# Performance work log

Hardware: AMD Instinct MI355X
Metric: run time of the kernel (lower is better)

## Reference

```python
import jax, jax.numpy as jnp
import numpy as np

N, E = 20000, 320000
CIN = 128; H = 128
EDGE_DIM = 16; SDIM = 3; KS = 3
K = KS ** SDIM          # 27 kernel weight matrices
S = 2 ** SDIM           # 8 non-zero B-spline taps per edge (degree-1)
MLP_HID = 2 * SDIM


def _glorot(key, shape, fan_in):
    return jax.random.normal(key, shape, dtype=jnp.float32) / np.sqrt(fan_in)


def setup_inputs() -> dict:
    key = jax.random.key(0)
    ks = jax.random.split(key, 16)
    inp = {
        "x": jax.random.normal(ks[0], (N, CIN), dtype=jnp.float32),
        "edge_index": jax.random.randint(ks[1], (2, E), 0, N, dtype=jnp.int64),
        "edge_attr": jax.random.normal(ks[2], (E, EDGE_DIM), dtype=jnp.float32),
        # edge preprocessor MLP
        "Wp1": _glorot(ks[3], (EDGE_DIM, MLP_HID), EDGE_DIM),
        "bp1": jnp.zeros((MLP_HID,), jnp.float32),
        "Wp2": _glorot(ks[4], (MLP_HID, SDIM), MLP_HID),
        "bp2": jnp.zeros((SDIM,), jnp.float32),
    }
    cins = [CIN, H, H]
    for l in range(3):
        inp[f"W{l}"] = _glorot(ks[5 + 3 * l], (K, cins[l], H), cins[l] * 2)
        inp[f"Wr{l}"] = _glorot(ks[6 + 3 * l], (cins[l], H), cins[l])
        inp[f"b{l}"] = jnp.zeros((H,), jnp.float32)
    return inp


def spline_basis(u):
    """Degree-1 open B-spline basis. u: [E, SDIM] in [0,1].
    Returns (weights [E,S], flat kernel indices [E,S])."""
    v = u * (KS - 1)
    lo = jnp.clip(jnp.floor(v), 0, KS - 2)
    frac = v - lo                      # [E, SDIM]
    lo = lo.astype(jnp.int32)
    ws, idxs = [], []
    for s in range(S):
        w = jnp.ones(u.shape[0], dtype=u.dtype)
        idx = jnp.zeros(u.shape[0], dtype=jnp.int32)
        stride = 1
        for d in range(SDIM):
            bit = (s >> d) & 1
            w = w * (frac[:, d] if bit else (1.0 - frac[:, d]))
            idx = idx + (lo[:, d] + bit) * stride
            stride *= KS
        ws.append(w); idxs.append(idx)
    return jnp.stack(ws, 1), jnp.stack(idxs, 1)


def spline_conv(x, src, dst, bw, bidx, W, Wr, b):
    """SplineConv with sum aggregation, root weight and bias."""
    cin = x.shape[1]
    x_src = x[src]                              # [E, Cin] gather
    T = jnp.zeros((N * K, cin), dtype=x.dtype)  # per-(node, kernel-idx) accumulator
    for s in range(S):                          # fixed small tap count
        seg = dst * K + bidx[:, s]              # [E]
        T = T + jax.ops.segment_sum(bw[:, s, None] * x_src, seg, num_segments=N * K)
    T = T.reshape(N, K, cin)
    return jnp.einsum('nki,kio->no', T, W) + x @ Wr + b


def reference(x, edge_index, edge_attr, Wp1, bp1, Wp2, bp2,
              W0, Wr0, b0, W1, Wr1, b1, W2, Wr2, b2):
    src = edge_index[0].astype(jnp.int32)
    dst = edge_index[1].astype(jnp.int32)
    # edge preprocessor MLP + sigmoid -> pseudo coords in (0,1)
    u = jax.nn.sigmoid(jax.nn.relu(edge_attr @ Wp1 + bp1) @ Wp2 + bp2)
    bw, bidx = spline_basis(u)
    h = spline_conv(x, src, dst, bw, bidx, W0, Wr0, b0)
    h = jax.nn.relu(h)  # dropout: eval mode (identity)
    h = spline_conv(h, src, dst, bw, bidx, W1, Wr1, b1)
    h = jax.nn.relu(h)
    h = spline_conv(h, src, dst, bw, bidx, W2, Wr2, b2)
    return h
```

## Files before the change

kernel.cpp:

```cpp
#include <hip/hip_runtime.h>
#include <hip/hip_bf16.h>
#include <hip/hip_fp16.h>

#define N_NODES 20000
#define E_EDGES 320000
#define CIN 128
#define HDIM 128
#define EDGE_DIM 16
#define SDIM 3
#define KS 3
#define KK 27
#define NB 28
#define KSTEPS 112
#define TLD (KK * 128)
#define WLD 28
#define MLP_HID 6

typedef __attribute__((ext_vector_type(8))) short v8s;
typedef __attribute__((ext_vector_type(4))) float v4f;
typedef unsigned short ush;

static __device__ __forceinline__ short f2bf(float v) {
    unsigned u = __float_as_uint(v);
    unsigned r = (u + 0x7fffu + ((u >> 16) & 1u)) >> 16;
    return (short)r;
}
static __device__ __forceinline__ float bf2f_lo(unsigned u) {
    return __uint_as_float(u << 16);
}
static __device__ __forceinline__ float bf2f_hi(unsigned u) {
    return __uint_as_float(u & 0xffff0000u);
}
static __device__ __forceinline__ unsigned pack2bf(float a, float b) {
    return ((unsigned)(ush)f2bf(a)) | (((unsigned)(ush)f2bf(b)) << 16);
}

__global__ void detect_kernel(const unsigned int* __restrict__ e, int* __restrict__ flag) {
    __shared__ int s_nz;
    if (threadIdx.x == 0) s_nz = 0;
    __syncthreads();
    unsigned int v = e[threadIdx.x * 2 + 1];
    if (v != 0) atomicAdd(&s_nz, 1);
    __syncthreads();
    if (threadIdx.x == 0) *flag = (s_nz > 0) ? 1 : 0;
}

__global__ void decode_edges(const void* __restrict__ eraw, const int* __restrict__ flag,
                             int* __restrict__ e32, int n) {
    int i = blockIdx.x * blockDim.x + threadIdx.x;
    if (i >= n) return;
    if (*flag) e32[i] = ((const int*)eraw)[i];
    else       e32[i] = (int)(((const long long*)eraw)[i]);
}

__global__ void edge_basis(const float* __restrict__ ea,
                           const float* __restrict__ Wp1, const float* __restrict__ bp1,
                           const float* __restrict__ Wp2, const float* __restrict__ bp2,
                           float4* __restrict__ fb) {
    __shared__ float sW1[EDGE_DIM * MLP_HID];
    __shared__ float sb1[MLP_HID];
    __shared__ float sW2[MLP_HID * SDIM];
    __shared__ float sb2[SDIM];
    int t = threadIdx.x;
    if (t < EDGE_DIM * MLP_HID) sW1[t] = Wp1[t];
    if (t < MLP_HID)            sb1[t] = bp1[t];
    if (t < MLP_HID * SDIM)     sW2[t] = Wp2[t];
    if (t < SDIM)               sb2[t] = bp2[t];
    __syncthreads();
    int e = blockIdx.x * blockDim.x + t;
    if (e >= E_EDGES) return;

    float a[EDGE_DIM];
#pragma unroll
    for (int i = 0; i < EDGE_DIM; i++) a[i] = ea[(long)e * EDGE_DIM + i];

    float hid[MLP_HID];
#pragma unroll
    for (int j = 0; j < MLP_HID; j++) {
        float s = sb1[j];
#pragma unroll
        for (int i = 0; i < EDGE_DIM; i++) s += a[i] * sW1[i * MLP_HID + j];
        hid[j] = fmaxf(s, 0.f);
    }

    float fr[SDIM];
    unsigned lp = 0;
#pragma unroll
    for (int d = 0; d < SDIM; d++) {
        float s = sb2[d];
#pragma unroll
        for (int j = 0; j < MLP_HID; j++) s += hid[j] * sW2[j * SDIM + d];
        float u = 1.f / (1.f + expf(-s));
        float v = u * (float)(KS - 1);
        float l = floorf(v);
        l = fminf(fmaxf(l, 0.f), (float)(KS - 2));
        fr[d] = v - l;
        lp |= ((unsigned)(int)l) << (8 * d);
    }
    float4 o;
    o.x = fr[0]; o.y = fr[1]; o.z = fr[2]; o.w = __uint_as_float(lp);
    fb[e] = o;
}

__global__ void zero_int(int* __restrict__ p, int n) {
    int i = blockIdx.x * blockDim.x + threadIdx.x;
    if (i < n) p[i] = 0;
}

__global__ void hist_kernel(const int* __restrict__ dst, int* __restrict__ hist) {
    int e = blockIdx.x * blockDim.x + threadIdx.x;
    if (e >= E_EDGES) return;
    atomicAdd(&hist[dst[e]], 1);
}

__global__ void scan_kernel(const int* __restrict__ hist, int* __restrict__ rowptr, int B) {
    __shared__ int part[256];
    int t = threadIdx.x;
    const int per = (B + 255) / 256;
    int base = t * per;
    int s = 0;
    for (int i = 0; i < per; i++) {
        int idx = base + i;
        if (idx < B) s += hist[idx];
    }
    part[t] = s;
    __syncthreads();
    for (int off = 1; off < 256; off <<= 1) {
        int v = (t >= off) ? part[t - off] : 0;
        __syncthreads();
        part[t] += v;
        __syncthreads();
    }
    int run = (t == 0) ? 0 : part[t - 1];
    for (int i = 0; i < per; i++) {
        int idx = base + i;
        if (idx < B) { rowptr[idx] = run; run += hist[idx]; }
    }
    if (t == 255) rowptr[B] = run;
}

__global__ void perm_kernel(const int* __restrict__ dst,
                            const int* __restrict__ rowptr, int* __restrict__ cursor,
                            int* __restrict__ eperm) {
    int e = blockIdx.x * blockDim.x + threadIdx.x;
    if (e >= E_EDGES) return;
    int bin = dst[e];
    int pos = rowptr[bin] + atomicAdd(&cursor[bin], 1);
    eperm[pos] = e;
}

__global__ void pack_w27(const int* __restrict__ eperm, const int* __restrict__ src,
                         const float4* __restrict__ fb,
                         int* __restrict__ srcp, float* __restrict__ w28p) {
    int j = blockIdx.x * blockDim.x + threadIdx.x;
    if (j >= E_EDGES) return;
    int e = eperm[j];
    srcp[j] = src[e];
    float4 f = fb[e];
    unsigned lp = __float_as_uint(f.w);
    float fr[3] = {f.x, f.y, f.z};
    float t[3][3];
#pragma unroll
    for (int d = 0; d < 3; d++) {
        int lo = (lp >> (8 * d)) & 255;
        float fd = fr[d];
#pragma unroll
        for (int q = 0; q < 3; q++)
            t[d][q] = (q == lo) ? (1.f - fd) : (q == lo + 1) ? fd : 0.f;
    }
    float out[WLD];
#pragma unroll
    for (int k2 = 0; k2 < 3; k2++)
#pragma unroll
        for (int k1 = 0; k1 < 3; k1++)
#pragma unroll
            for (int k0 = 0; k0 < 3; k0++)
                out[k2 * 9 + k1 * 3 + k0] = t[0][k0] * t[1][k1] * t[2][k2];
    out[27] = 0.f;
    float* op = w28p + (size_t)j * WLD;
#pragma unroll
    for (int q = 0; q < WLD / 4; q++) *(float4*)(op + 4 * q) = *(float4*)(out + 4 * q);
}

__global__ void packW3_kernel(const float* __restrict__ W0, const float* __restrict__ Wr0,
                              const float* __restrict__ W1, const float* __restrict__ Wr1,
                              const float* __restrict__ W2, const float* __restrict__ Wr2,
                              short* __restrict__ hi) {
    int gid = blockIdx.x * blockDim.x + threadIdx.x;
    if (gid >= 3 * NB * 4 * 8 * 64) return;
    int lane = gid & 63;
    int nt = (gid >> 6) & 7;
    int ks = (gid >> 9) & 3;
    int kb2 = gid >> 11;
    int layer = kb2 / NB;
    int kb = kb2 - layer * NB;
    const float* W  = (layer == 0) ? W0  : (layer == 1) ? W1  : W2;
    const float* Wr = (layer == 0) ? Wr0 : (layer == 1) ? Wr1 : Wr2;
    int i0 = ks * 32 + ((lane >> 4) & 3) * 8;
    int o = nt * 16 + (lane & 15);
    const float* src = (kb < KK) ? (W + (long)kb * 16384 + (long)i0 * 128 + o)
                                 : (Wr + (long)i0 * 128 + o);
    long off = ((long)(((size_t)layer * NB + kb) * 4 + ks) * 8 + nt) * 64 * 8
             + (long)lane * 8;
#pragma unroll
    for (int j = 0; j < 8; j++) {
        float v = src[(long)j * 128];
        hi[off + j] = f2bf(v);
    }
}

__global__ void conv_xb(const float* __restrict__ x, ush* __restrict__ xb) {
    int i = blockIdx.x * blockDim.x + threadIdx.x;
    if (i >= N_NODES * CIN / 4) return;
    float4 v = ((const float4*)x)[i];
    uint2 d;
    d.x = pack2bf(v.x, v.y);
    d.y = pack2bf(v.z, v.w);
    ((uint2*)xb)[i] = d;
}

__global__ __launch_bounds__(64) void accumT_kernel(
    const ush* __restrict__ act, const int* __restrict__ rowptr,
    const int* __restrict__ srcp, const float* __restrict__ w28p,
    ush* __restrict__ T, int n0)
{
    int lane = threadIdx.x;
    int n = n0 + blockIdx.x;
    int jb = rowptr[n], je = rowptr[n + 1];

    float acc[KK][2];
#pragma unroll
    for (int k = 0; k < KK; k++) { acc[k][0] = 0.f; acc[k][1] = 0.f; }

    const ush* actl = act + lane * 2;
    const float4* w4 = (const float4*)w28p;

    if (jb < je) {
        int last = je - 1;
        int j1 = (jb + 1 > last) ? last : jb + 1;
        int j2 = (jb + 2 > last) ? last : jb + 2;
        int j3 = (jb + 3 > last) ? last : jb + 3;
        unsigned x0c = *(const unsigned*)(actl + (size_t)srcp[jb] * 128);
        unsigned x1c = *(const unsigned*)(actl + (size_t)j1 * 0 + (size_t)srcp[j1] * 128);
        float4 w0c[7], w1c[7];
#pragma unroll
        for (int q = 0; q < 7; q++) w0c[q] = w4[(size_t)jb * 7 + q];
#pragma unroll
        for (int q = 0; q < 7; q++) w1c[q] = w4[(size_t)j1 * 7 + q];
        int s0n = srcp[j2];
        int s1n = srcp[j3];

        for (int j = jb; j < je; j += 2) {
            {
                float x0 = bf2f_lo(x0c), x1 = bf2f_hi(x0c);
                float w[28];
#pragma unroll
                for (int q = 0; q < 7; q++) *(float4*)(w + 4 * q) = w0c[q];
#pragma unroll
                for (int k = 0; k < KK; k++) {
                    acc[k][0] += w[k] * x0;
                    acc[k][1] += w[k] * x1;
                }
            }
            {
                int jn = (j + 2 > last) ? last : j + 2;
                x0c = *(const unsigned*)(actl + (size_t)s0n * 128);
#pragma unroll
                for (int q = 0; q < 7; q++) w0c[q] = w4[(size_t)jn * 7 + q];
                int jf = (j + 4 > last) ? last : j + 4;
                s0n = srcp[jf];
            }
            if (j + 1 < je) {
                {
                    float x0 = bf2f_lo(x1c), x1 = bf2f_hi(x1c);
                    float w[28];
#pragma unroll
                    for (int q = 0; q < 7; q++) *(float4*)(w + 4 * q) = w1c[q];
#pragma unroll
                    for (int k = 0; k < KK; k++) {
                        acc[k][0] += w[k] * x0;
                        acc[k][1] += w[k] * x1;
                    }
                }
                int jn = (j + 3 > last) ? last : j + 3;
                x1c = *(const unsigned*)(actl + (size_t)s1n * 128);
#pragma unroll
                for (int q = 0; q < 7; q++) w1c[q] = w4[(size_t)jn * 7 + q];
                int jf = (j + 5 > last) ? last : j + 5;
                s1n = srcp[jf];
            }
        }
    }

    ush* tp = T + (size_t)(n - n0) * TLD + lane * 2;
#pragma unroll
    for (int k = 0; k < KK; k++) {
        *(unsigned*)(tp + (size_t)k * 128) = pack2bf(acc[k][0], acc[k][1]);
    }
}

__global__ __launch_bounds__(512) void gemm2_kernel(
    const ush* __restrict__ T, const ush* __restrict__ act,
    const short* __restrict__ Wh, const float* __restrict__ bias,
    ush* __restrict__ actout, float* __restrict__ fout,
    int n0, int relu)
{
    __shared__ float S[512][17];
    int lane = threadIdx.x & 63;
    int wave = threadIdx.x >> 6;
    int mtr = blockIdx.x;

    v4f acc[8];
#pragma unroll
    for (int nt = 0; nt < 8; nt++) acc[nt] = (v4f){0.f, 0.f, 0.f, 0.f};

    int arow = mtr * 16 + (lane & 15);
    int sub  = (lane >> 4) & 3;
    const ush* tp = T + (size_t)arow * TLD + sub * 8;
    const ush* ap = act + (size_t)(n0 + arow) * 128 + sub * 8;

    int ks0 = wave * (KSTEPS / 8);
#pragma unroll
    for (int i = 0; i < KSTEPS / 8; i++) {
        int ks = ks0 + i;
        v8s a = (ks < KK * 4) ? *(const v8s*)(tp + ks * 32)
                              : *(const v8s*)(ap + (ks - KK * 4) * 32);
        const short* wb = Wh + (size_t)ks * 4096 + (size_t)lane * 8;
#pragma unroll
        for (int nt = 0; nt < 8; nt++) {
            v8s b = *(const v8s*)(wb + (size_t)nt * 512);
            acc[nt] = __builtin_amdgcn_mfma_f32_16x16x32_bf16(a, b, acc[nt], 0, 0, 0);
        }
    }

    int r  = threadIdx.x >> 5;
    int cl = (threadIdx.x & 31) * 2;
    int row = n0 + mtr * 16 + r;
#pragma unroll
    for (int p = 0; p < 2; p++) {
        __syncthreads();
#pragma unroll
        for (int q = 0; q < 16; q++) S[threadIdx.x][q] = acc[p * 4 + (q >> 2)][q & 3];
        __syncthreads();
        float v[2];
#pragma unroll
        for (int h = 0; h < 2; h++) {
            int c = p * 64 + cl + h;
            int ln  = (c & 15) + 16 * (r >> 2);
            int idx = (((c & 63) >> 4) << 2) + (r & 3);
            float s = 0.f;
#pragma unroll
            for (int w = 0; w < 8; w++) s += S[w * 64 + ln][idx];
            s += bias[c];
            if (relu) s = fmaxf(s, 0.f);
            v[h] = s;
        }
        int c0 = p * 64 + cl;
        if (actout) {
            *(unsigned*)(actout + (size_t)row * 128 + c0) = pack2bf(v[0], v[1]);
        } else {
            float2 f2; f2.x = v[0]; f2.y = v[1];
            *(float2*)(fout + (size_t)row * 128 + c0) = f2;
        }
    }
}

extern "C" void kernel_launch(void* const* d_in, const int* in_sizes, int n_in,
                              void* d_out, int out_size, void* d_ws, size_t ws_size,
                              hipStream_t stream) {
    const float* x   = (const float*)d_in[0];
    const void*  eix = d_in[1];
    const float* ea  = (const float*)d_in[2];
    const float* Wp1 = (const float*)d_in[3];
    const float* bp1 = (const float*)d_in[4];
    const float* Wp2 = (const float*)d_in[5];
    const float* bp2 = (const float*)d_in[6];
    const float* W[3]  = {(const float*)d_in[7],  (const float*)d_in[10], (const float*)d_in[13]};
    const float* Wr[3] = {(const float*)d_in[8],  (const float*)d_in[11], (const float*)d_in[14]};
    const float* b[3]  = {(const float*)d_in[9],  (const float*)d_in[12], (const float*)d_in[15]};
    float* out = (float*)d_out;

    char* ws = (char*)d_ws;
    size_t off = 0;
    auto walloc = [&](size_t bytes) -> void* {
        void* p = ws + off;
        off = (off + bytes + 255) & ~(size_t)255;
        return p;
    };
    int*    flag    = (int*)   walloc(sizeof(int));
    int*    e32     = (int*)   walloc(sizeof(int) * 2 * E_EDGES);
    float4* fb      = (float4*)walloc(sizeof(float4) * (size_t)E_EDGES);
    int*    srcp    = (int*)   walloc(sizeof(int) * E_EDGES);
    int*    eperm   = (int*)   walloc(sizeof(int) * E_EDGES);
    float*  w28p    = (float*) walloc(sizeof(float) * (size_t)E_EDGES * WLD);
    int*    histcur = (int*)   walloc(sizeof(int) * (size_t)N_NODES * 2);
    int*    rowptr  = (int*)   walloc(sizeof(int) * (N_NODES + 1));
    ush*    xb      = (ush*)   walloc(sizeof(ush) * (size_t)N_NODES * 128);
    ush*    a1      = (ush*)   walloc(sizeof(ush) * (size_t)N_NODES * 128);
    ush*    a2      = (ush*)   walloc(sizeof(ush) * (size_t)N_NODES * 128);
    short*  Wh3     = (short*) walloc(sizeof(short) * (size_t)3 * NB * 128 * 128);

    int chunk_n = 10000;
    {
        const int cand[3] = {10000, 4000, 2000};
        for (int i = 0; i < 3; i++) {
            size_t need = (size_t)cand[i] * TLD * sizeof(ush);
            chunk_n = cand[i];
            if (off + need <= ws_size) break;
        }
    }
    ush* T = (ush*)walloc((size_t)chunk_n * TLD * sizeof(ush));

    int* srcv = e32;
    int* dstv = e32 + E_EDGES;
    int* hist   = histcur;
    int* cursor = histcur + N_NODES;

    detect_kernel<<<1, 1024, 0, stream>>>((const unsigned int*)eix, flag);
    decode_edges<<<(2 * E_EDGES + 255) / 256, 256, 0, stream>>>(eix, flag, e32, 2 * E_EDGES);
    edge_basis<<<(E_EDGES + 255) / 256, 256, 0, stream>>>(ea, Wp1, bp1, Wp2, bp2, fb);

    zero_int<<<(N_NODES * 2 + 255) / 256, 256, 0, stream>>>(histcur, N_NODES * 2);
    hist_kernel<<<(E_EDGES + 255) / 256, 256, 0, stream>>>(dstv, hist);
    scan_kernel<<<1, 256, 0, stream>>>(hist, rowptr, N_NODES);
    perm_kernel<<<(E_EDGES + 255) / 256, 256, 0, stream>>>(dstv, rowptr, cursor, eperm);
    pack_w27<<<(E_EDGES + 255) / 256, 256, 0, stream>>>(eperm, srcv, fb, srcp, w28p);

    packW3_kernel<<<(3 * NB * 4 * 8 * 64 + 255) / 256, 256, 0, stream>>>(
        W[0], Wr[0], W[1], Wr[1], W[2], Wr[2], Wh3);
    conv_xb<<<(N_NODES * CIN / 4 + 255) / 256, 256, 0, stream>>>(x, xb);

    const ush* actin = xb;
    for (int l = 0; l < 3; l++) {
        const short* Wh = Wh3 + (size_t)l * NB * 128 * 128;
        ush* actout = (l == 0) ? a1 : (l == 1) ? a2 : nullptr;
        for (int n0 = 0; n0 < N_NODES; n0 += chunk_n) {
            int cn = (n0 + chunk_n <= N_NODES) ? chunk_n : (N_NODES - n0);
            int nmt = cn / 16;
            accumT_kernel<<<cn, 64, 0, stream>>>(actin, rowptr, srcp, w28p, T, n0);
            gemm2_kernel<<<nmt, 512, 0, stream>>>(
                T, actin, Wh, b[l], actout, (l == 2) ? out : nullptr,
                n0, (l < 2) ? 1 : 0);
        }
        if (l == 0) actin = a1; else if (l == 1) actin = a2;
    }
}
```

Baseline: 620.0 us.

## Fuse per-node T accumulation with MFMA GEMM via LDS tile; parallelize scan

Merges the accumT and gemm2 kernels into one kernel per 16-node tile. Each of the 8 waves accumulates two nodes' 27x128 T rows into padded LDS, and the MFMA GEMM then reads T from LDS instead of a global buffer. This removes the large global write and read-back of T and the chunked launches. It also replaces the single-block prefix scan with a three-kernel hierarchical scan. The cost is about 110KB of LDS plus a float staging buffer per block, which limits occupancy to roughly one block per CU, and the gather phase now shares a block with the GEMM.

```diff
diff --git a/kernel.cpp b/kernel.cpp
--- a/kernel.cpp
+++ b/kernel.cpp
@@ -12,8 +12,8 @@
 #define KK 27
 #define NB 28
 #define KSTEPS 112
-#define TLD (KK * 128)
 #define WLD 28
+#define TLDS 3464
 #define MLP_HID 6
 
 typedef __attribute__((ext_vector_type(8))) short v8s;
@@ -113,30 +113,41 @@
     atomicAdd(&hist[dst[e]], 1);
 }
 
-__global__ void scan_kernel(const int* __restrict__ hist, int* __restrict__ rowptr, int B) {
-    __shared__ int part[256];
-    int t = threadIdx.x;
-    const int per = (B + 255) / 256;
-    int base = t * per;
-    int s = 0;
-    for (int i = 0; i < per; i++) {
-        int idx = base + i;
-        if (idx < B) s += hist[idx];
-    }
-    part[t] = s;
+__global__ void scan_blk(const int* __restrict__ hist, int* __restrict__ rowptr,
+                         int* __restrict__ bsum, int B) {
+    __shared__ int sh[256];
+    int i = blockIdx.x * 256 + threadIdx.x;
+    int v = (i < B) ? hist[i] : 0;
+    sh[threadIdx.x] = v;
     __syncthreads();
     for (int off = 1; off < 256; off <<= 1) {
-        int v = (t >= off) ? part[t - off] : 0;
-        __syncthreads();
-        part[t] += v;
-        __syncthreads();
-    }
-    int run = (t == 0) ? 0 : part[t - 1];
-    for (int i = 0; i < per; i++) {
-        int idx = base + i;
-        if (idx < B) { rowptr[idx] = run; run += hist[idx]; }
-    }
-    if (t == 255) rowptr[B] = run;
+        int t = (threadIdx.x >= off) ? sh[threadIdx.x - off] : 0;
+        __syncthreads();
+        sh[threadIdx.x] += t;
+        __syncthreads();
+    }
+    if (i < B) rowptr[i] = sh[threadIdx.x] - v;
+    if (threadIdx.x == 255) bsum[blockIdx.x] = sh[255];
+}
+
+__global__ void scan_top(int* __restrict__ bsum, int nb) {
+    __shared__ int sh[256];
+    int v = (threadIdx.x < nb) ? bsum[threadIdx.x] : 0;
+    sh[threadIdx.x] = v;
+    __syncthreads();
+    for (int off = 1; off < 256; off <<= 1) {
+        int t = (threadIdx.x >= off) ? sh[threadIdx.x - off] : 0;
+        __syncthreads();
+        sh[threadIdx.x] += t;
+        __syncthreads();
+    }
+    if (threadIdx.x < nb) bsum[threadIdx.x] = sh[threadIdx.x] - v;
+}
+
+__global__ void scan_add(int* __restrict__ rowptr, const int* __restrict__ bsum, int B) {
+    int i = blockIdx.x * 256 + threadIdx.x;
+    if (i < B) rowptr[i] += bsum[blockIdx.x];
+    if (i == 0) rowptr[B] = E_EDGES;
 }
 
 __global__ void perm_kernel(const int* __restrict__ dst,
@@ -219,128 +230,126 @@
     ((uint2*)xb)[i] = d;
 }
 
-__global__ __launch_bounds__(64) void accumT_kernel(
+__global__ __launch_bounds__(512) void fused_kernel(
     const ush* __restrict__ act, const int* __restrict__ rowptr,
     const int* __restrict__ srcp, const float* __restrict__ w28p,
-    ush* __restrict__ T, int n0)
+    const short* __restrict__ Wh, const float* __restrict__ bias,
+    ush* __restrict__ actout, float* __restrict__ fout, int relu)
 {
-    int lane = threadIdx.x;
-    int n = n0 + blockIdx.x;
-    int jb = rowptr[n], je = rowptr[n + 1];
-
-    float acc[KK][2];
-#pragma unroll
-    for (int k = 0; k < KK; k++) { acc[k][0] = 0.f; acc[k][1] = 0.f; }
+    __shared__ ush Tl[16 * TLDS];
+    __shared__ float S[512][17];
+    int lane = threadIdx.x & 63;
+    int wave = threadIdx.x >> 6;
 
     const ush* actl = act + lane * 2;
     const float4* w4 = (const float4*)w28p;
 
-    if (jb < je) {
-        int last = je - 1;
-        int j1 = (jb + 1 > last) ? last : jb + 1;
-        int j2 = (jb + 2 > last) ? last : jb + 2;
-        int j3 = (jb + 3 > last) ? last : jb + 3;
-        unsigned x0c = *(const unsigned*)(actl + (size_t)srcp[jb] * 128);
-        unsigned x1c = *(const unsigned*)(actl + (size_t)j1 * 0 + (size_t)srcp[j1] * 128);
-        float4 w0c[7], w1c[7];
-#pragma unroll
-        for (int q = 0; q < 7; q++) w0c[q] = w4[(size_t)jb * 7 + q];
-#pragma unroll
-        for (int q = 0; q < 7; q++) w1c[q] = w4[(size_t)j1 * 7 + q];
-        int s0n = srcp[j2];
-        int s1n = srcp[j3];
-
-        for (int j = jb; j < je; j += 2) {
-            {
-                float x0 = bf2f_lo(x0c), x1 = bf2f_hi(x0c);
-                float w[28];
-#pragma unroll
-                for (int q = 0; q < 7; q++) *(float4*)(w + 4 * q) = w0c[q];
-#pragma unroll
-                for (int k = 0; k < KK; k++) {
-                    acc[k][0] += w[k] * x0;
-                    acc[k][1] += w[k] * x1;
-                }
-            }
-            {
-                int jn = (j + 2 > last) ? last : j + 2;
-                x0c = *(const unsigned*)(actl + (size_t)s0n * 128);
-#pragma unroll
-                for (int q = 0; q < 7; q++) w0c[q] = w4[(size_t)jn * 7 + q];
-                int jf = (j + 4 > last) ? last : j + 4;
-                s0n = srcp[jf];
-            }
-            if (j + 1 < je) {
+#pragma unroll
+    for (int half = 0; half < 2; half++) {
+        int idx = wave + half * 8;
+        int n = blockIdx.x * 16 + idx;
+        int jb = rowptr[n], je = rowptr[n + 1];
+
+        float acc[KK][2];
+#pragma unroll
+        for (int k = 0; k < KK; k++) { acc[k][0] = 0.f; acc[k][1] = 0.f; }
+
+        if (jb < je) {
+            int last = je - 1;
+            int j1 = (jb + 1 > last) ? last : jb + 1;
+            int j2 = (jb + 2 > last) ? last : jb + 2;
+            int j3 = (jb + 3 > last) ? last : jb + 3;
+            unsigned x0c = *(const unsigned*)(actl + (size_t)srcp[jb] * 128);
+            unsigned x1c = *(const unsigned*)(actl + (size_t)srcp[j1] * 128);
+            float4 w0c[7], w1c[7];
+#pragma unroll
+            for (int q = 0; q < 7; q++) w0c[q] = w4[(size_t)jb * 7 + q];
+#pragma unroll
+            for (int q = 0; q < 7; q++) w1c[q] = w4[(size_t)j1 * 7 + q];
+            int s0n = srcp[j2];
+            int s1n = srcp[j3];
+
+            for (int j = jb; j < je; j += 2) {
                 {
-                    float x0 = bf2f_lo(x1c), x1 = bf2f_hi(x1c);
+                    float x0 = bf2f_lo(x0c), x1 = bf2f_hi(x0c);
                     float w[28];
 #pragma unroll
-                    for (int q = 0; q < 7; q++) *(float4*)(w + 4 * q) = w1c[q];
+                    for (int q = 0; q < 7; q++) *(float4*)(w + 4 * q) = w0c[q];
 #pragma unroll
                     for (int k = 0; k < KK; k++) {
                         acc[k][0] += w[k] * x0;
                         acc[k][1] += w[k] * x1;
                     }
                 }
-                int jn = (j + 3 > last) ? last : j + 3;
-                x1c = *(const unsigned*)(actl + (size_t)s1n * 128);
-#pragma unroll
-                for (int q = 0; q < 7; q++) w1c[q] = w4[(size_t)jn * 7 + q];
-                int jf = (j + 5 > last) ? last : j + 5;
-                s1n = srcp[jf];
+                {
+                    int jn = (j + 2 > last) ? last : j + 2;
+                    x0c = *(const unsigned*)(actl + (size_t)s0n * 128);
+#pragma unroll
+                    for (int q = 0; q < 7; q++) w0c[q] = w4[(size_t)jn * 7 + q];
+                    int jf = (j + 4 > last) ? last : j + 4;
+                    s0n = srcp[jf];
+                }
+                if (j + 1 < je) {
+                    {
+                        float x0 = bf2f_lo(x1c), x1 = bf2f_hi(x1c);
+                        float w[28];
+#pragma unroll
+                        for (int q = 0; q < 7; q++) *(float4*)(w + 4 * q) = w1c[q];
+#pragma unroll
+                        for (int k = 0; k < KK; k++) {
+                            acc[k][0] += w[k] * x0;
+                            acc[k][1] += w[k] * x1;
+                        }
+                    }
+                    int jn = (j + 3 > last) ? last : j + 3;
+                    x1c = *(const unsigned*)(actl + (size_t)s1n * 128);
+#pragma unroll
+                    for (int q = 0; q < 7; q++) w1c[q] = w4[(size_t)jn * 7 + q];
+                    int jf = (j + 5 > last) ? last : j + 5;
+                    s1n = srcp[jf];
+                }
             }
         }
-    }
-
-    ush* tp = T + (size_t)(n - n0) * TLD + lane * 2;
-#pragma unroll
-    for (int k = 0; k < KK; k++) {
-        *(unsigned*)(tp + (size_t)k * 128) = pack2bf(acc[k][0], acc[k][1]);
-    }
-}
-
-__global__ __launch_bounds__(512) void gemm2_kernel(
-    const ush* __restrict__ T, const ush* __restrict__ act,
-    const short* __restrict__ Wh, const float* __restrict__ bias,
-    ush* __restrict__ actout, float* __restrict__ fout,
-    int n0, int relu)
-{
-    __shared__ float S[512][17];
-    int lane = threadIdx.x & 63;
-    int wave = threadIdx.x >> 6;
-    int mtr = blockIdx.x;
-
-    v4f acc[8];
-#pragma unroll
-    for (int nt = 0; nt < 8; nt++) acc[nt] = (v4f){0.f, 0.f, 0.f, 0.f};
-
-    int arow = mtr * 16 + (lane & 15);
-    int sub  = (lane >> 4) & 3;
-    const ush* tp = T + (size_t)arow * TLD + sub * 8;
-    const ush* ap = act + (size_t)(n0 + arow) * 128 + sub * 8;
+
+        ush* tp = Tl + idx * TLDS + lane * 2;
+#pragma unroll
+        for (int k = 0; k < KK; k++)
+            *(unsigned*)(tp + k * 128) = pack2bf(acc[k][0], acc[k][1]);
+    }
+
+    __syncthreads();
+
+    v4f acc2[8];
+#pragma unroll
+    for (int nt = 0; nt < 8; nt++) acc2[nt] = (v4f){0.f, 0.f, 0.f, 0.f};
+
+    int r15 = lane & 15;
+    int sub = (lane >> 4) & 3;
+    const ush* tl = Tl + r15 * TLDS + sub * 8;
+    const ush* ap = act + (size_t)(blockIdx.x * 16 + r15) * 128 + sub * 8;
 
     int ks0 = wave * (KSTEPS / 8);
 #pragma unroll
     for (int i = 0; i < KSTEPS / 8; i++) {
         int ks = ks0 + i;
-        v8s a = (ks < KK * 4) ? *(const v8s*)(tp + ks * 32)
+        v8s a = (ks < KK * 4) ? *(const v8s*)(tl + ks * 32)
                               : *(const v8s*)(ap + (ks - KK * 4) * 32);
         const short* wb = Wh + (size_t)ks * 4096 + (size_t)lane * 8;
 #pragma unroll
         for (int nt = 0; nt < 8; nt++) {
             v8s b = *(const v8s*)(wb + (size_t)nt * 512);
-            acc[nt] = __builtin_amdgcn_mfma_f32_16x16x32_bf16(a, b, acc[nt], 0, 0, 0);
+            acc2[nt] = __builtin_amdgcn_mfma_f32_16x16x32_bf16(a, b, acc2[nt], 0, 0, 0);
         }
     }
 
     int r  = threadIdx.x >> 5;
     int cl = (threadIdx.x & 31) * 2;
-    int row = n0 + mtr * 16 + r;
+    int row = blockIdx.x * 16 + r;
 #pragma unroll
     for (int p = 0; p < 2; p++) {
         __syncthreads();
 #pragma unroll
-        for (int q = 0; q < 16; q++) S[threadIdx.x][q] = acc[p * 4 + (q >> 2)][q & 3];
+        for (int q = 0; q < 16; q++) S[threadIdx.x][q] = acc2[p * 4 + (q >> 2)][q & 3];
         __syncthreads();
         float v[2];
 #pragma unroll
@@ -395,21 +404,12 @@
     float*  w28p    = (float*) walloc(sizeof(float) * (size_t)E_EDGES * WLD);
     int*    histcur = (int*)   walloc(sizeof(int) * (size_t)N_NODES * 2);
     int*    rowptr  = (int*)   walloc(sizeof(int) * (N_NODES + 1));
+    int*    bsum    = (int*)   walloc(sizeof(int) * 256);
     ush*    xb      = (ush*)   walloc(sizeof(ush) * (size_t)N_NODES * 128);
     ush*    a1      = (ush*)   walloc(sizeof(ush) * (size_t)N_NODES * 128);
     ush*    a2      = (ush*)   walloc(sizeof(ush) * (size_t)N_NODES * 128);
     short*  Wh3     = (short*) walloc(sizeof(short) * (size_t)3 * NB * 128 * 128);
-
-    int chunk_n = 10000;
-    {
-        const int cand[3] = {10000, 4000, 2000};
-        for (int i = 0; i < 3; i++) {
-            size_t need = (size_t)cand[i] * TLD * sizeof(ush);
-            chunk_n = cand[i];
-            if (off + need <= ws_size) break;
-        }
-    }
-    ush* T = (ush*)walloc((size_t)chunk_n * TLD * sizeof(ush));
+    (void)ws_size;
 
     int* srcv = e32;
     int* dstv = e32 + E_EDGES;
@@ -420,9 +420,12 @@
     decode_edges<<<(2 * E_EDGES + 255) / 256, 256, 0, stream>>>(eix, flag, e32, 2 * E_EDGES);
     edge_basis<<<(E_EDGES + 255) / 256, 256, 0, stream>>>(ea, Wp1, bp1, Wp2, bp2, fb);
 
+    const int NBLK = (N_NODES + 255) / 256;
     zero_int<<<(N_NODES * 2 + 255) / 256, 256, 0, stream>>>(histcur, N_NODES * 2);
     hist_kernel<<<(E_EDGES + 255) / 256, 256, 0, stream>>>(dstv, hist);
-    scan_kernel<<<1, 256, 0, stream>>>(hist, rowptr, N_NODES);
+    scan_blk<<<NBLK, 256, 0, stream>>>(hist, rowptr, bsum, N_NODES);
+    scan_top<<<1, 256, 0, stream>>>(bsum, NBLK);
+    scan_add<<<NBLK, 256, 0, stream>>>(rowptr, bsum, N_NODES);
     perm_kernel<<<(E_EDGES + 255) / 256, 256, 0, stream>>>(dstv, rowptr, cursor, eperm);
     pack_w27<<<(E_EDGES + 255) / 256, 256, 0, stream>>>(eperm, srcv, fb, srcp, w28p);
 
@@ -434,14 +437,9 @@
     for (int l = 0; l < 3; l++) {
         const short* Wh = Wh3 + (size_t)l * NB * 128 * 128;
         ush* actout = (l == 0) ? a1 : (l == 1) ? a2 : nullptr;
-        for (int n0 = 0; n0 < N_NODES; n0 += chunk_n) {
-            int cn = (n0 + chunk_n <= N_NODES) ? chunk_n : (N_NODES - n0);
-            int nmt = cn / 16;
-            accumT_kernel<<<cn, 64, 0, stream>>>(actin, rowptr, srcp, w28p, T, n0);
-            gemm2_kernel<<<nmt, 512, 0, stream>>>(
-                T, actin, Wh, b[l], actout, (l == 2) ? out : nullptr,
-                n0, (l < 2) ? 1 : 0);
-        }
+        fused_kernel<<<N_NODES / 16, 512, 0, stream>>>(
+            actin, rowptr, srcp, w28p, Wh, b[l], actout,
+            (l == 2) ? out : nullptr, (l < 2) ? 1 : 0);
         if (l == 0) actin = a1; else if (l == 1) actin = a2;
     }
 }
```

After: 654.2 us. +5.5%, slower.
